# Optimization experiments

Hardware: AMD Instinct MI355X
Metric: run time of the kernel (lower is better)

## Reference

```python
import jax, jax.numpy as jnp
import numpy as np

B, P, K, L, F_NR, KS, NC = 32, 2048, 16, 8, 64, 5, 40
N = B * P
EPS = 1e-5


def setup_inputs() -> dict:
    key = jax.random.key(0)
    ks = jax.random.split(key, 6)
    pos = jax.random.normal(ks[0], (N, 3), jnp.float32)
    batch = jnp.repeat(jnp.arange(B, dtype=jnp.int32), P)
    # SplineConv(1, F_NR, dim=3, kernel_size=KS): weight [KS^3, in=1, out] flattened to [KS^3, F]
    w_spline = jax.random.normal(ks[1], (KS ** 3, F_NR), jnp.float32) * 0.1
    w_root = jax.random.normal(ks[2], (F_NR,), jnp.float32) * 0.1
    b_spline = jnp.zeros((F_NR,), jnp.float32)
    bn_gamma = jnp.ones((F_NR,), jnp.float32)
    bn_beta = jnp.zeros((F_NR,), jnp.float32)
    w1 = jax.random.normal(ks[3], (F_NR, 256), jnp.float32) / np.sqrt(F_NR).astype(np.float32)
    b1 = jnp.zeros((256,), jnp.float32)
    w2 = jax.random.normal(ks[4], (256, NC), jnp.float32) / np.sqrt(256).astype(np.float32)
    b2 = jnp.zeros((NC,), jnp.float32)
    return dict(pos=pos, batch=batch, w_spline=w_spline, w_root=w_root,
                b_spline=b_spline, bn_gamma=bn_gamma, bn_beta=bn_beta,
                w1=w1, b1=b1, w2=w2, b2=b2)


def _knn_one_cloud(pb):  # pb: [P,3] -> k nearest neighbor indices [P,K] (no self loops)
    sq = jnp.sum(pb * pb, axis=-1)
    d = sq[:, None] + sq[None, :] - 2.0 * (pb @ pb.T)
    d = jnp.where(jnp.eye(P, dtype=bool), jnp.inf, d)
    _, idx = jax.lax.top_k(-d, K)
    return idx


def reference(pos, batch, w_spline, w_root, b_spline, bn_gamma, bn_beta, w1, b1, w2, b2):
    # --- knn_graph, grouped k-per-center ---
    posb = pos.reshape(B, P, 3)
    nbr = jax.vmap(_knn_one_cloud)(posb)                          # [B,P,K] local
    nbr = (nbr + (jnp.arange(B) * P)[:, None, None]).reshape(N, K)
    clusters = pos[nbr] - pos[:, None, :]                          # [N,K,3]
    # --- per-point 3x3 covariance over first L neighbors ---
    cl = clusters[:, :L, :]
    cov = jnp.einsum('nlc,nld->ncd', cl, cl)                       # [N,3,3]
    # --- diag(): 5 iterations of batched QR iteration; rows of V = eigenvectors ---
    A = cov
    Vt = jnp.broadcast_to(jnp.eye(3, dtype=pos.dtype), (N, 3, 3))
    for _ in range(5):
        Q, R = jnp.linalg.qr(A)
        A = R @ Q
        Vt = Vt @ Q
    V = jnp.swapaxes(Vt, 1, 2)                                     # [N,3,3]
    # --- rotate clusters into eigenbasis: clusters @ V^T ---
    dc = jnp.einsum('nkc,ndc->nkd', clusters, V)                   # [N,K,3]
    signs = jnp.sign(jnp.sum(dc[:, :, 2], axis=1))
    dc = dc.at[:, :, 2].multiply(signs[:, None])
    max_abs = jnp.max(jnp.abs(dc).reshape(N, K * 3), axis=1)
    dc = dc / max_abs[:, None, None] * 0.5 + 0.5                   # pseudo coords in [0,1]
    # --- SplineConv (degree-1 open B-splines, dim=3): x_j = 1, aggr='mean' ---
    p = dc * (KS - 1)
    i0 = jnp.clip(jnp.floor(p), 0, KS - 2).astype(jnp.int32)       # [N,K,3]
    f = p - i0                                                     # fractional part
    acc = jnp.zeros((N, K, F_NR), pos.dtype)
    for c in range(8):                                             # 8 corners of trilinear basis
        bits = [(c >> d) & 1 for d in range(3)]
        kidx = sum((i0[..., d] + bits[d]) * (KS ** d) for d in range(3))
        w = jnp.ones((N, K), pos.dtype)
        for d in range(3):
            w = w * (f[..., d] if bits[d] else 1.0 - f[..., d])
        acc = acc + w[..., None] * w_spline[kidx]                  # [N,K,F]
    out_nondir = acc.mean(axis=1) + w_root + b_spline              # root*x_i + bias, x_i = 1
    # --- BatchNorm1d (training-mode batch stats, biased var) ---
    mu = out_nondir.mean(axis=0)
    var = out_nondir.var(axis=0)
    y = (out_nondir - mu) / jnp.sqrt(var + EPS) * bn_gamma + bn_beta
    # --- head ---
    y = jax.nn.sigmoid(y)
    ys = y.reshape(B, P, F_NR).mean(axis=1)                        # [B,F]
    y1 = jax.nn.elu(ys @ w1 + b1)
    y2 = jax.nn.log_softmax(y1 @ w2 + b2, axis=1)
    return y2
```

## Files before the change

kernel.cpp:

```cpp
#include <hip/hip_runtime.h>
#include <math.h>

#define B_ 32
#define P_ 2048
#define N_ 65536
#define K_ 16
#define L_ 8
#define F_ 64
#define KS_ 5
#define KS3_ 125
#define NC_ 40
#define H_ 256
#define EPS_ 1e-5f
#define QPB_ 64
#define SEG_ 4
#define SEGLEN_ 512

__device__ __forceinline__ float distf(float4 C, float nx, float ny, float nz, float qs) {
    return fmaf(C.x, nx, fmaf(C.y, ny, fmaf(C.z, nz, C.w))) + qs;
}

#define CES(a, b) { unsigned _mn = min(a, b); b = max(a, b); a = _mn; }

__device__ __forceinline__ void sort8(unsigned& e0, unsigned& e1, unsigned& e2, unsigned& e3,
                                      unsigned& e4, unsigned& e5, unsigned& e6, unsigned& e7) {
    CES(e0, e1) CES(e2, e3) CES(e4, e5) CES(e6, e7)
    CES(e0, e2) CES(e1, e3) CES(e4, e6) CES(e5, e7)
    CES(e1, e2) CES(e5, e6)
    CES(e0, e4) CES(e1, e5) CES(e2, e6) CES(e3, e7)
    CES(e2, e4) CES(e3, e5)
    CES(e1, e2) CES(e3, e4) CES(e5, e6)
}

__device__ __forceinline__ void bitmerge16(unsigned (&a)[16]) {
#pragma unroll
    for (int dd = 8; dd >= 1; dd >>= 1)
#pragma unroll
        for (int k2 = 0; k2 < 16; k2 += 2 * dd)
#pragma unroll
            for (int i2 = k2; i2 < k2 + dd; i2++)
                CES(a[i2], a[i2 + dd])
}

__device__ __forceinline__ void sort16(unsigned (&a)[16]) {
    sort8(a[0], a[1], a[2], a[3], a[4], a[5], a[6], a[7]);
    sort8(a[8], a[9], a[10], a[11], a[12], a[13], a[14], a[15]);
    unsigned t;
    t = a[8];  a[8]  = a[15]; a[15] = t;
    t = a[9];  a[9]  = a[14]; a[14] = t;
    t = a[10]; a[10] = a[13]; a[13] = t;
    t = a[11]; a[11] = a[12]; a[12] = t;
    bitmerge16(a);
}

__device__ __forceinline__ void flush8(unsigned (&bu)[16],
                                       unsigned& e0, unsigned& e1, unsigned& e2, unsigned& e3,
                                       unsigned& e4, unsigned& e5, unsigned& e6, unsigned& e7,
                                       unsigned& thr) {
    sort8(e0, e1, e2, e3, e4, e5, e6, e7);
    CES(bu[8],  e7) CES(bu[9],  e6) CES(bu[10], e5) CES(bu[11], e4)
    CES(bu[12], e3) CES(bu[13], e2) CES(bu[14], e1) CES(bu[15], e0)
    bitmerge16(bu);
    e0 = e1 = e2 = e3 = e4 = e5 = e6 = e7 = 0xFFFFFFFFu;
    unsigned t16 = bu[15];
    t16 = min(t16, (unsigned)__shfl_xor((int)t16, 1, 64));
    t16 = min(t16, (unsigned)__shfl_xor((int)t16, 2, 64));
    thr = min(thr, t16);
}

__global__ __launch_bounds__(256, 4) void knn_geom_kernel(const float* __restrict__ pos,
                                                          float* __restrict__ dcn) {
    __shared__ float4 cloud[P_];
    int b = blockIdx.x >> 5, tile = blockIdx.x & 31;
    int base = b * P_;
    int t = threadIdx.x;
    for (int j = t; j < P_; j += 256) {
        float x = pos[(base + j) * 3 + 0];
        float y = pos[(base + j) * 3 + 1];
        float z = pos[(base + j) * 3 + 2];
        cloud[j] = make_float4(x, y, z, x * x + y * y + z * z);
    }
    __syncthreads();

    int s = t & 3;
    int il = tile * QPB_ + (t >> 2);
    float4 Q = cloud[il];
    float nx = -2.f * Q.x, ny = -2.f * Q.y, nz = -2.f * Q.z, qs = Q.w;

    int j0 = s << 9, off = s << 1;

    unsigned bu[16];
#pragma unroll
    for (int m = 0; m < 16; m++) {
        int j_ = j0 | ((m + off) & 511);
        float4 Cv = cloud[j_];
        float d_ = distf(Cv, nx, ny, nz, qs);
        bu[m] = (__float_as_uint(fmaxf(d_, 0.f)) & 0xFFFFF800u) | (unsigned)j_;
    }
    sort16(bu);
    unsigned thr;
    {
        unsigned t16 = bu[15];
        t16 = min(t16, (unsigned)__shfl_xor((int)t16, 1, 64));
        t16 = min(t16, (unsigned)__shfl_xor((int)t16, 2, 64));
        thr = t16;
    }

    unsigned e0 = ~0u, e1 = ~0u, e2 = ~0u, e3 = ~0u,
             e4 = ~0u, e5 = ~0u, e6 = ~0u, e7 = ~0u;

#define VISIT(Cv, JJ) {                                                          \
        int j_ = j0 | (((JJ) + off) & 511);                                      \
        float d_ = distf(Cv, nx, ny, nz, qs);                                    \
        unsigned key_ = (__float_as_uint(fmaxf(d_, 0.f)) & 0xFFFFF800u)          \
                        | (unsigned)j_;                                          \
        bool a_ = (key_ < thr);                                                  \
        e7 = a_ ? e6 : e7;  e6 = a_ ? e5 : e6;  e5 = a_ ? e4 : e5;               \
        e4 = a_ ? e3 : e4;  e3 = a_ ? e2 : e3;  e2 = a_ ? e1 : e2;               \
        e1 = a_ ? e0 : e1;  e0 = a_ ? key_ : e0;                                 \
    }

    float4 c0 = cloud[j0 | ((16 + off) & 511)];
    float4 c1 = cloud[j0 | ((17 + off) & 511)];
    float4 c2 = cloud[j0 | ((18 + off) & 511)];
    float4 c3 = cloud[j0 | ((19 + off) & 511)];
    for (int jj = 16; jj < SEGLEN_; jj += 4) {
        float4 n0 = cloud[j0 | ((jj + off + 4) & 511)];
        float4 n1 = cloud[j0 | ((jj + off + 5) & 511)];
        float4 n2 = cloud[j0 | ((jj + off + 6) & 511)];
        float4 n3 = cloud[j0 | ((jj + off + 7) & 511)];
        VISIT(c0, jj + 0)
        VISIT(c1, jj + 1)
        VISIT(c2, jj + 2)
        VISIT(c3, jj + 3)
        if (__any(e4 != 0xFFFFFFFFu))
            flush8(bu, e0, e1, e2, e3, e4, e5, e6, e7, thr);
        c0 = n0; c1 = n1; c2 = n2; c3 = n3;
    }
    flush8(bu, e0, e1, e2, e3, e4, e5, e6, e7, thr);
#undef VISIT

    {
        bool own = (s == (il >> 9));
#pragma unroll
        for (int m = 0; m < 15; m++) bu[m] = own ? bu[m + 1] : bu[m];
        bu[15] = own ? 0xFFFFFFFFu : bu[15];
    }

#pragma unroll
    for (int mask = 1; mask <= 2; mask <<= 1) {
        unsigned o[16];
#pragma unroll
        for (int i = 0; i < 16; i++)
            o[i] = (unsigned)__shfl_xor((int)bu[15 - i], mask, 64);
#pragma unroll
        for (int i = 0; i < 16; i++) bu[i] = min(bu[i], o[i]);
        bitmerge16(bu);
    }

    int mi[16];
#pragma unroll
    for (int m = 0; m < 16; m++) mi[m] = bu[m] & 0x7FF;

    float px = Q.x, py = Q.y, pz = Q.z;
    float A[3][3];
    {
        float a00 = 0, a01 = 0, a02 = 0, a11 = 0, a12 = 0, a22 = 0;
#pragma unroll
        for (int l = 0; l < L_; l++) {
            float4 Cv = cloud[mi[l]];
            float ccx = Cv.x - px, ccy = Cv.y - py, ccz = Cv.z - pz;
            a00 += ccx * ccx; a01 += ccx * ccy; a02 += ccx * ccz;
            a11 += ccy * ccy; a12 += ccy * ccz; a22 += ccz * ccz;
        }
        A[0][0] = a00; A[0][1] = a01; A[0][2] = a02;
        A[1][0] = a01; A[1][1] = a11; A[1][2] = a12;
        A[2][0] = a02; A[2][1] = a12; A[2][2] = a22;
    }
    float Vt[3][3] = {{1.f, 0.f, 0.f}, {0.f, 1.f, 0.f}, {0.f, 0.f, 1.f}};

    for (int it = 0; it < 5; it++) {
        float M00 = A[0][0], M01 = A[0][1], M02 = A[0][2];
        float M10 = A[1][0], M11 = A[1][1], M12 = A[1][2];
        float M20 = A[2][0], M21 = A[2][1], M22 = A[2][2];
        float tau0 = 0.f, v1 = 0.f, v2 = 0.f;
        float xn2 = M10 * M10 + M20 * M20;
        if (xn2 != 0.f) {
            float beta = -copysignf(sqrtf(M00 * M00 + xn2), M00);
            tau0 = (beta - M00) / beta;
            float inv = 1.f / (M00 - beta);
            v1 = M10 * inv; v2 = M20 * inv;
            float sc;
            sc = tau0 * (M01 + v1 * M11 + v2 * M21); M01 -= sc; M11 -= v1 * sc; M21 -= v2 * sc;
            sc = tau0 * (M02 + v1 * M12 + v2 * M22); M02 -= sc; M12 -= v1 * sc; M22 -= v2 * sc;
            M00 = beta;
        }
        float tau1 = 0.f, u2 = 0.f;
        if (M21 != 0.f) {
            float beta1 = -copysignf(sqrtf(M11 * M11 + M21 * M21), M11);
            tau1 = (beta1 - M11) / beta1;
            u2 = M21 / (M11 - beta1);
            float sc = tau1 * (M12 + u2 * M22); M12 -= sc; M22 -= u2 * sc;
            M11 = beta1;
        }
        float h11 = 1.f - tau1, h12 = -tau1 * u2, h22 = 1.f - tau1 * u2 * u2;
        float Qm[3][3];
        Qm[0][0] = 1.f - tau0;
        Qm[1][0] = -v1 * tau0;
        Qm[2][0] = -v2 * tau0;
        float t1 = tau0 * (v1 * h11 + v2 * h12);
        Qm[0][1] = -t1;
        Qm[1][1] = h11 - v1 * t1;
        Qm[2][1] = h12 - v2 * t1;
        float t2 = tau0 * (v1 * h12 + v2 * h22);
        Qm[0][2] = -t2;
        Qm[1][2] = h12 - v1 * t2;
        Qm[2][2] = h22 - v2 * t2;
        A[0][0] = M00 * Qm[0][0] + M01 * Qm[1][0] + M02 * Qm[2][0];
        A[0][1] = M00 * Qm[0][1] + M01 * Qm[1][1] + M02 * Qm[2][1];
        A[0][2] = M00 * Qm[0][2] + M01 * Qm[1][2] + M02 * Qm[2][2];
        A[1][0] = M11 * Qm[1][0] + M12 * Qm[2][0];
        A[1][1] = M11 * Qm[1][1] + M12 * Qm[2][1];
        A[1][2] = M11 * Qm[1][2] + M12 * Qm[2][2];
        A[2][0] = M22 * Qm[2][0];
        A[2][1] = M22 * Qm[2][1];
        A[2][2] = M22 * Qm[2][2];
        float nv[3][3];
#pragma unroll
        for (int r = 0; r < 3; r++)
#pragma unroll
            for (int cc = 0; cc < 3; cc++)
                nv[r][cc] = Vt[r][0] * Qm[0][cc] + Vt[r][1] * Qm[1][cc] + Vt[r][2] * Qm[2][cc];
#pragma unroll
        for (int r = 0; r < 3; r++)
#pragma unroll
            for (int cc = 0; cc < 3; cc++) Vt[r][cc] = nv[r][cc];
    }

    float s2 = 0.f, mx01 = 0.f, mx2 = 0.f;
#pragma unroll
    for (int k = 0; k < K_; k++) {
        float4 Cv = cloud[mi[k]];
        float ccx = Cv.x - px, ccy = Cv.y - py, ccz = Cv.z - pz;
        float d0 = ccx * Vt[0][0] + ccy * Vt[1][0] + ccz * Vt[2][0];
        float d1 = ccx * Vt[0][1] + ccy * Vt[1][1] + ccz * Vt[2][1];
        float d2 = ccx * Vt[0][2] + ccy * Vt[1][2] + ccz * Vt[2][2];
        s2 += d2;
        mx01 = fmaxf(mx01, fmaxf(fabsf(d0), fabsf(d1)));
        mx2  = fmaxf(mx2, fabsf(d2));
    }
    float sg = (s2 > 0.f) ? 1.f : ((s2 < 0.f) ? -1.f : 0.f);
    float mx = fmaxf(mx01, (sg == 0.f) ? 0.f : mx2);
    float hs = 0.5f / mx;

    {
        int i = base + il;
        float4* row = (float4*)(dcn + (size_t)i * 48);
        int g = s;
        float v[12];
#pragma unroll
        for (int kk = 0; kk < 4; kk++) {
            int k = g * 4 + kk;
            float4 Cv = cloud[mi[k]];
            float ccx = Cv.x - px, ccy = Cv.y - py, ccz = Cv.z - pz;
            float d0 = ccx * Vt[0][0] + ccy * Vt[1][0] + ccz * Vt[2][0];
            float d1 = ccx * Vt[0][1] + ccy * Vt[1][1] + ccz * Vt[2][1];
            float d2 = (ccx * Vt[0][2] + ccy * Vt[1][2] + ccz * Vt[2][2]) * sg;
            v[kk * 3 + 0] = d0 * hs + 0.5f;
            v[kk * 3 + 1] = d1 * hs + 0.5f;
            v[kk * 3 + 2] = d2 * hs + 0.5f;
        }
#pragma unroll
        for (int r = 0; r < 3; r++)
            row[g * 3 + r] = make_float4(v[r * 4 + 0], v[r * 4 + 1],
                                         v[r * 4 + 2], v[r * 4 + 3]);
    }
}

__global__ __launch_bounds__(256) void spline_kernel(const float* __restrict__ dcn,
                                                     const float* __restrict__ w_spline,
                                                     const float* __restrict__ w_root,
                                                     const float* __restrict__ b_spline,
                                                     float* __restrict__ x,
                                                     float* __restrict__ partials) {
    __shared__ float ws_t[F_ * KS3_];
    __shared__ float red[4][64];
    {
        int f = threadIdx.x & 63;
        for (int c = threadIdx.x >> 6; c < KS3_; c += 4)
            ws_t[f * KS3_ + c] = w_spline[c * 64 + f];
    }
    __syncthreads();
    int wave = threadIdx.x >> 6, f = threadIdx.x & 63;
    const float* wbase = &ws_t[f * KS3_];
    float wr = w_root[f] + b_spline[f];
    float s1 = 0.f, s2 = 0.f;
    for (int p = 0; p < 16; p++) {
        int i = blockIdx.x * 64 + wave * 16 + p;
        const float4* row = (const float4*)(dcn + (size_t)i * 48);
        float pr[48];
#pragma unroll
        for (int m = 0; m < 12; m++) {
            float4 v = row[m];
            pr[m * 4 + 0] = v.x; pr[m * 4 + 1] = v.y;
            pr[m * 4 + 2] = v.z; pr[m * 4 + 3] = v.w;
        }
        float acc = 0.f;
#pragma unroll
        for (int k = 0; k < K_; k++) {
            float p0 = pr[k * 3 + 0] * 4.f;
            float p1 = pr[k * 3 + 1] * 4.f;
            float p2 = pr[k * 3 + 2] * 4.f;
            float i0 = fminf(fmaxf(floorf(p0), 0.f), 3.f);
            float i1 = fminf(fmaxf(floorf(p1), 0.f), 3.f);
            float i2 = fminf(fmaxf(floorf(p2), 0.f), 3.f);
            float f0 = p0 - i0, f1 = p1 - i1, f2 = p2 - i2;
            float g0 = 1.f - f0, g1 = 1.f - f1, g2 = 1.f - f2;
            int c = (int)fmaf(i2, 25.f, fmaf(i1, 5.f, i0));
            const float* wp = wbase + c;
            float a0 = wp[0],  a1 = wp[1];
            float b0 = wp[5],  b1v = wp[6];
            float c0 = wp[25], c1 = wp[26];
            float d0 = wp[30], d1 = wp[31];
            float wA = g1 * g2, wB = f1 * g2, wC = g1 * f2, wD = f1 * f2;
            acc = fmaf(wA, fmaf(f0, a1, g0 * a0), acc);
            acc = fmaf(wB, fmaf(f0, b1v, g0 * b0), acc);
            acc = fmaf(wC, fmaf(f0, c1, g0 * c0), acc);
            acc = fmaf(wD, fmaf(f0, d1, g0 * d0), acc);
        }
        float xv = acc * (1.f / 16.f) + wr;
        x[(size_t)i * 64 + f] = xv;
        s1 += xv; s2 += xv * xv;
    }
    red[wave][f] = s1; __syncthreads();
    if (threadIdx.x < 64)
        partials[blockIdx.x * 128 + f] = red[0][f] + red[1][f] + red[2][f] + red[3][f];
    __syncthreads();
    red[wave][f] = s2; __syncthreads();
    if (threadIdx.x < 64)
        partials[blockIdx.x * 128 + 64 + f] = red[0][f] + red[1][f] + red[2][f] + red[3][f];
}

__global__ __launch_bounds__(256) void stats_kernel(const float* __restrict__ partials,
                                                    const float* __restrict__ gamma,
                                                    const float* __restrict__ beta,
                                                    float* __restrict__ stats) {
    __shared__ double red1[256], red2[256];
    int t = threadIdx.x;
    int f = t & 63, g = t >> 6;
    double a0 = 0, a1 = 0, a2 = 0, a3 = 0, q0 = 0, q1 = 0, q2 = 0, q3 = 0;
    for (int b2 = g; b2 < 1024; b2 += 16) {
        a0 += (double)partials[(b2     ) * 128 + f];
        q0 += (double)partials[(b2     ) * 128 + 64 + f];
        a1 += (double)partials[(b2 +  4) * 128 + f];
        q1 += (double)partials[(b2 +  4) * 128 + 64 + f];
        a2 += (double)partials[(b2 +  8) * 128 + f];
        q2 += (double)partials[(b2 +  8) * 128 + 64 + f];
        a3 += (double)partials[(b2 + 12) * 128 + f];
        q3 += (double)partials[(b2 + 12) * 128 + 64 + f];
    }
    red1[t] = (a0 + a1) + (a2 + a3);
    red2[t] = (q0 + q1) + (q2 + q3);
    __syncthreads();
    if (t < 64) {
        double S1 = red1[t] + red1[t + 64] + red1[t + 128] + red1[t + 192];
        double S2 = red2[t] + red2[t + 64] + red2[t + 128] + red2[t + 192];
        double mu = S1 / (double)N_;
        double var = S2 / (double)N_ - mu * mu;
        double scale = (double)gamma[t] / sqrt(var + (double)EPS_);
        double shift = (double)beta[t] - mu * scale;
        stats[t] = (float)scale;
        stats[64 + t] = (float)shift;
    }
}

__global__ __launch_bounds__(256) void pool_partial_kernel(const float* __restrict__ x,
                                                           const float* __restrict__ stats,
                                                           float* __restrict__ pp) {
    __shared__ float red[4][64];
    int blk = blockIdx.x;
    int b = blk >> 5, ch = blk & 31;
    int f = threadIdx.x & 63, w = threadIdx.x >> 6;
    float scale = stats[f], shift = stats[64 + f];
    float acc = 0.f;
    int row0 = b * P_ + ch * 64;
    for (int r = w; r < 64; r += 4) {
        float v = x[(size_t)(row0 + r) * 64 + f];
        float t = fmaf(v, scale, shift);
        acc += __fdividef(1.f, 1.f + __expf(-t));
    }
    red[w][f] = acc; __syncthreads();
    if (threadIdx.x < 64) pp[blk * 64 + f] = red[0][f] + red[1][f] + red[2][f] + red[3][f];
}

__global__ __launch_bounds__(256) void mlp1_kernel(const float* __restrict__ pp,
                                                   const float* __restrict__ w1,
                                                   const float* __restrict__ b1,
                                                   float* __restrict__ y1) {
    __shared__ float ssy[64];
    int b = blockIdx.x, t = threadIdx.x;
    if (t < 64) {
        float s = 0.f;
#pragma unroll
        for (int g = 0; g < 32; g++) s += pp[(b * 32 + g) * 64 + t];
        ssy[t] = s * (1.f / 2048.f);
    }
    __syncthreads();
    float acc = b1[t];
#pragma unroll 8
    for (int c = 0; c < F_; c++) acc = fmaf(ssy[c], w1[c * 256 + t], acc);
    y1[b * 256 + t] = acc > 0.f ? acc : expm1f(acc);
}

__global__ __launch_bounds__(64) void mlp2_kernel(const float* __restrict__ y1,
                                                  const float* __restrict__ w2,
                                                  const float* __restrict__ b2,
                                                  float* __restrict__ out) {
    int b = blockIdx.x, j = threadIdx.x;
    float acc = -INFINITY;
    if (j < NC_) {
        acc = b2[j];
#pragma unroll 8
        for (int c = 0; c < H_; c++) acc = fmaf(y1[b * 256 + c], w2[c * 40 + j], acc);
    }
    float m = acc;
#pragma unroll
    for (int o = 32; o > 0; o >>= 1) m = fmaxf(m, __shfl_xor(m, o, 64));
    float e = (j < NC_) ? expf(acc - m) : 0.f;
    float s = e;
#pragma unroll
    for (int o = 32; o > 0; o >>= 1) s += __shfl_xor(s, o, 64);
    if (j < NC_) out[b * NC_ + j] = acc - m - logf(s);
}

extern "C" void kernel_launch(void* const* d_in, const int* in_sizes, int n_in,
                              void* d_out, int out_size, void* d_ws, size_t ws_size,
                              hipStream_t stream) {
    const float* pos      = (const float*)d_in[0];
    const float* w_spline = (const float*)d_in[2];
    const float* w_root   = (const float*)d_in[3];
    const float* b_spline = (const float*)d_in[4];
    const float* bn_gamma = (const float*)d_in[5];
    const float* bn_beta  = (const float*)d_in[6];
    const float* w1       = (const float*)d_in[7];
    const float* b1       = (const float*)d_in[8];
    const float* w2       = (const float*)d_in[9];
    const float* b2       = (const float*)d_in[10];
    float* out = (float*)d_out;

    char* ws = (char*)d_ws;
    float* dcn      = (float*)(ws + 0);
    float* x        = (float*)(ws + (12u << 20));
    float* partials = (float*)(ws + (28u << 20));
    float* stats    = (float*)(ws + (28u << 20) + (512u << 10));
    float* pp       = (float*)(ws + (28u << 20) + (512u << 10) + 4096);
    float* y1       = (float*)(ws + (28u << 20) + (512u << 10) + 4096 + (256u << 10));

    knn_geom_kernel<<<B_ * 32, 256, 0, stream>>>(pos, dcn);
    spline_kernel<<<N_ / 64, 256, 0, stream>>>(dcn, w_spline, w_root, b_spline, x, partials);
    stats_kernel<<<1, 256, 0, stream>>>(partials, bn_gamma, bn_beta, stats);
    pool_partial_kernel<<<B_ * 32, 256, 0, stream>>>(x, stats, pp);
    mlp1_kernel<<<B_, 256, 0, stream>>>(pp, w1, b1, y1);
    mlp2_kernel<<<B_, 64, 0, stream>>>(y1, w2, b2, out);
}
```

Measured before the change: 208.1 us.

## Linearize kNN scan addressing with padded cloud and fuse MLP head kernels

The kNN scan loop drops the masked wraparound index computation. It walks a linear pointer with a tail that handles the wrapped-around start elements under predication, and pads the shared cloud with sentinel points so reads past the segment stay in bounds. The neighbor index array is removed in favor of masking the sorted keys directly, and the output projection is rewritten without a temp array. The two small MLP kernels are fused into one so the hidden activations stay in shared memory, which removes a launch and a global round trip. The tail logic adds complexity and risks edge-case errors in how the wrapped elements are covered.

Measured after the change: 192.1 us. -7.7%, faster.

```diff
diff --git a/kernel.cpp b/kernel.cpp
--- a/kernel.cpp
+++ b/kernel.cpp
@@ -14,7 +14,6 @@
 #define EPS_ 1e-5f
 #define QPB_ 64
 #define SEG_ 4
-#define SEGLEN_ 512
 
 __device__ __forceinline__ float distf(float4 C, float nx, float ny, float nz, float qs) {
     return fmaf(C.x, nx, fmaf(C.y, ny, fmaf(C.z, nz, C.w))) + qs;
@@ -70,7 +69,7 @@
 
 __global__ __launch_bounds__(256, 4) void knn_geom_kernel(const float* __restrict__ pos,
                                                           float* __restrict__ dcn) {
-    __shared__ float4 cloud[P_];
+    __shared__ float4 cloud[P_ + 8];
     int b = blockIdx.x >> 5, tile = blockIdx.x & 31;
     int base = b * P_;
     int t = threadIdx.x;
@@ -80,6 +79,7 @@
         float z = pos[(base + j) * 3 + 2];
         cloud[j] = make_float4(x, y, z, x * x + y * y + z * z);
     }
+    if (t < 8) cloud[P_ + t] = make_float4(0.f, 0.f, 0.f, 1e30f);
     __syncthreads();
 
     int s = t & 3;
@@ -92,7 +92,7 @@
     unsigned bu[16];
 #pragma unroll
     for (int m = 0; m < 16; m++) {
-        int j_ = j0 | ((m + off) & 511);
+        int j_ = j0 + off + m;
         float4 Cv = cloud[j_];
         float d_ = distf(Cv, nx, ny, nz, qs);
         bu[m] = (__float_as_uint(fmaxf(d_, 0.f)) & 0xFFFFF800u) | (unsigned)j_;
@@ -109,36 +109,71 @@
     unsigned e0 = ~0u, e1 = ~0u, e2 = ~0u, e3 = ~0u,
              e4 = ~0u, e5 = ~0u, e6 = ~0u, e7 = ~0u;
 
-#define VISIT(Cv, JJ) {                                                          \
-        int j_ = j0 | (((JJ) + off) & 511);                                      \
+#define VISITL(Cv, Jv) {                                                         \
         float d_ = distf(Cv, nx, ny, nz, qs);                                    \
         unsigned key_ = (__float_as_uint(fmaxf(d_, 0.f)) & 0xFFFFF800u)          \
-                        | (unsigned)j_;                                          \
+                        | (unsigned)(Jv);                                        \
         bool a_ = (key_ < thr);                                                  \
         e7 = a_ ? e6 : e7;  e6 = a_ ? e5 : e6;  e5 = a_ ? e4 : e5;               \
         e4 = a_ ? e3 : e4;  e3 = a_ ? e2 : e3;  e2 = a_ ? e1 : e2;               \
         e1 = a_ ? e0 : e1;  e0 = a_ ? key_ : e0;                                 \
     }
-
-    float4 c0 = cloud[j0 | ((16 + off) & 511)];
-    float4 c1 = cloud[j0 | ((17 + off) & 511)];
-    float4 c2 = cloud[j0 | ((18 + off) & 511)];
-    float4 c3 = cloud[j0 | ((19 + off) & 511)];
-    for (int jj = 16; jj < SEGLEN_; jj += 4) {
-        float4 n0 = cloud[j0 | ((jj + off + 4) & 511)];
-        float4 n1 = cloud[j0 | ((jj + off + 5) & 511)];
-        float4 n2 = cloud[j0 | ((jj + off + 6) & 511)];
-        float4 n3 = cloud[j0 | ((jj + off + 7) & 511)];
-        VISIT(c0, jj + 0)
-        VISIT(c1, jj + 1)
-        VISIT(c2, jj + 2)
-        VISIT(c3, jj + 3)
+#define VISITP(Cv, Jv, P) {                                                      \
+        float d_ = distf(Cv, nx, ny, nz, qs);                                    \
+        unsigned key_ = (__float_as_uint(fmaxf(d_, 0.f)) & 0xFFFFF800u)          \
+                        | (unsigned)(Jv);                                        \
+        bool a_ = (key_ < thr) && (P);                                           \
+        e7 = a_ ? e6 : e7;  e6 = a_ ? e5 : e6;  e5 = a_ ? e4 : e5;               \
+        e4 = a_ ? e3 : e4;  e3 = a_ ? e2 : e3;  e2 = a_ ? e1 : e2;               \
+        e1 = a_ ? e0 : e1;  e0 = a_ ? key_ : e0;                                 \
+    }
+
+    const float4* cp = &cloud[j0 + off + 16];
+    int jc = j0 + off + 16;
+    for (int v = 0; v < 488; v += 4) {
+        float4 a0 = cp[v + 0], a1 = cp[v + 1], a2 = cp[v + 2], a3 = cp[v + 3];
+        VISITL(a0, jc + 0)
+        VISITL(a1, jc + 1)
+        VISITL(a2, jc + 2)
+        VISITL(a3, jc + 3)
+        jc += 4;
         if (__any(e4 != 0xFFFFFFFFu))
             flush8(bu, e0, e1, e2, e3, e4, e5, e6, e7, thr);
-        c0 = n0; c1 = n1; c2 = n2; c3 = n3;
+    }
+    {
+        int vlim = 496 - off;
+#pragma unroll
+        for (int v = 488; v < 492; v++) {
+            float4 a0 = cp[v];
+            VISITP(a0, jc, v < vlim) jc++;
+        }
+        if (__any(e4 != 0xFFFFFFFFu))
+            flush8(bu, e0, e1, e2, e3, e4, e5, e6, e7, thr);
+#pragma unroll
+        for (int v = 492; v < 496; v++) {
+            float4 a0 = cp[v];
+            VISITP(a0, jc, v < vlim) jc++;
+        }
+        if (__any(e4 != 0xFFFFFFFFu))
+            flush8(bu, e0, e1, e2, e3, e4, e5, e6, e7, thr);
+    }
+    {
+#pragma unroll
+        for (int u = 0; u < 4; u++) {
+            float4 a0 = cloud[j0 + u];
+            VISITP(a0, j0 + u, u < off)
+        }
+        if (__any(e4 != 0xFFFFFFFFu))
+            flush8(bu, e0, e1, e2, e3, e4, e5, e6, e7, thr);
+#pragma unroll
+        for (int u = 4; u < 6; u++) {
+            float4 a0 = cloud[j0 + u];
+            VISITP(a0, j0 + u, u < off)
+        }
     }
     flush8(bu, e0, e1, e2, e3, e4, e5, e6, e7, thr);
-#undef VISIT
+#undef VISITL
+#undef VISITP
 
     {
         bool own = (s == (il >> 9));
@@ -158,17 +193,13 @@
         bitmerge16(bu);
     }
 
-    int mi[16];
-#pragma unroll
-    for (int m = 0; m < 16; m++) mi[m] = bu[m] & 0x7FF;
-
     float px = Q.x, py = Q.y, pz = Q.z;
     float A[3][3];
     {
         float a00 = 0, a01 = 0, a02 = 0, a11 = 0, a12 = 0, a22 = 0;
 #pragma unroll
         for (int l = 0; l < L_; l++) {
-            float4 Cv = cloud[mi[l]];
+            float4 Cv = cloud[bu[l] & 0x7FF];
             float ccx = Cv.x - px, ccy = Cv.y - py, ccz = Cv.z - pz;
             a00 += ccx * ccx; a01 += ccx * ccy; a02 += ccx * ccz;
             a11 += ccy * ccy; a12 += ccy * ccz; a22 += ccz * ccz;
@@ -240,7 +271,7 @@
     float s2 = 0.f, mx01 = 0.f, mx2 = 0.f;
 #pragma unroll
     for (int k = 0; k < K_; k++) {
-        float4 Cv = cloud[mi[k]];
+        float4 Cv = cloud[bu[k] & 0x7FF];
         float ccx = Cv.x - px, ccy = Cv.y - py, ccz = Cv.z - pz;
         float d0 = ccx * Vt[0][0] + ccy * Vt[1][0] + ccz * Vt[2][0];
         float d1 = ccx * Vt[0][1] + ccy * Vt[1][1] + ccz * Vt[2][1];
@@ -257,23 +288,29 @@
         int i = base + il;
         float4* row = (float4*)(dcn + (size_t)i * 48);
         int g = s;
-        float v[12];
-#pragma unroll
-        for (int kk = 0; kk < 4; kk++) {
-            int k = g * 4 + kk;
-            float4 Cv = cloud[mi[k]];
-            float ccx = Cv.x - px, ccy = Cv.y - py, ccz = Cv.z - pz;
-            float d0 = ccx * Vt[0][0] + ccy * Vt[1][0] + ccz * Vt[2][0];
-            float d1 = ccx * Vt[0][1] + ccy * Vt[1][1] + ccz * Vt[2][1];
-            float d2 = (ccx * Vt[0][2] + ccy * Vt[1][2] + ccz * Vt[2][2]) * sg;
-            v[kk * 3 + 0] = d0 * hs + 0.5f;
-            v[kk * 3 + 1] = d1 * hs + 0.5f;
-            v[kk * 3 + 2] = d2 * hs + 0.5f;
-        }
-#pragma unroll
-        for (int r = 0; r < 3; r++)
-            row[g * 3 + r] = make_float4(v[r * 4 + 0], v[r * 4 + 1],
-                                         v[r * 4 + 2], v[r * 4 + 3]);
+        float4 Cv0 = cloud[bu[g * 4 + 0] & 0x7FF];
+        float4 Cv1 = cloud[bu[g * 4 + 1] & 0x7FF];
+        float4 Cv2 = cloud[bu[g * 4 + 2] & 0x7FF];
+        float4 Cv3 = cloud[bu[g * 4 + 3] & 0x7FF];
+        float x0 = Cv0.x - px, y0 = Cv0.y - py, z0 = Cv0.z - pz;
+        float x1 = Cv1.x - px, y1 = Cv1.y - py, z1 = Cv1.z - pz;
+        float x2 = Cv2.x - px, y2 = Cv2.y - py, z2 = Cv2.z - pz;
+        float x3 = Cv3.x - px, y3 = Cv3.y - py, z3 = Cv3.z - pz;
+        float p00 = (x0 * Vt[0][0] + y0 * Vt[1][0] + z0 * Vt[2][0]) * hs + 0.5f;
+        float p01 = (x0 * Vt[0][1] + y0 * Vt[1][1] + z0 * Vt[2][1]) * hs + 0.5f;
+        float p02 = (x0 * Vt[0][2] + y0 * Vt[1][2] + z0 * Vt[2][2]) * sg * hs + 0.5f;
+        float p10 = (x1 * Vt[0][0] + y1 * Vt[1][0] + z1 * Vt[2][0]) * hs + 0.5f;
+        float p11 = (x1 * Vt[0][1] + y1 * Vt[1][1] + z1 * Vt[2][1]) * hs + 0.5f;
+        float p12 = (x1 * Vt[0][2] + y1 * Vt[1][2] + z1 * Vt[2][2]) * sg * hs + 0.5f;
+        float p20 = (x2 * Vt[0][0] + y2 * Vt[1][0] + z2 * Vt[2][0]) * hs + 0.5f;
+        float p21 = (x2 * Vt[0][1] + y2 * Vt[1][1] + z2 * Vt[2][1]) * hs + 0.5f;
+        float p22 = (x2 * Vt[0][2] + y2 * Vt[1][2] + z2 * Vt[2][2]) * sg * hs + 0.5f;
+        float p30 = (x3 * Vt[0][0] + y3 * Vt[1][0] + z3 * Vt[2][0]) * hs + 0.5f;
+        float p31 = (x3 * Vt[0][1] + y3 * Vt[1][1] + z3 * Vt[2][1]) * hs + 0.5f;
+        float p32 = (x3 * Vt[0][2] + y3 * Vt[1][2] + z3 * Vt[2][2]) * sg * hs + 0.5f;
+        row[g * 3 + 0] = make_float4(p00, p01, p02, p10);
+        row[g * 3 + 1] = make_float4(p11, p12, p20, p21);
+        row[g * 3 + 2] = make_float4(p22, p30, p31, p32);
     }
 }
 
@@ -393,11 +430,14 @@
     if (threadIdx.x < 64) pp[blk * 64 + f] = red[0][f] + red[1][f] + red[2][f] + red[3][f];
 }
 
-__global__ __launch_bounds__(256) void mlp1_kernel(const float* __restrict__ pp,
-                                                   const float* __restrict__ w1,
-                                                   const float* __restrict__ b1,
-                                                   float* __restrict__ y1) {
+__global__ __launch_bounds__(256) void mlp_kernel(const float* __restrict__ pp,
+                                                  const float* __restrict__ w1,
+                                                  const float* __restrict__ b1,
+                                                  const float* __restrict__ w2,
+                                                  const float* __restrict__ b2,
+                                                  float* __restrict__ out) {
     __shared__ float ssy[64];
+    __shared__ float sy1[256];
     int b = blockIdx.x, t = threadIdx.x;
     if (t < 64) {
         float s = 0.f;
@@ -406,31 +446,30 @@
         ssy[t] = s * (1.f / 2048.f);
     }
     __syncthreads();
-    float acc = b1[t];
+    {
+        float acc = b1[t];
 #pragma unroll 8
-    for (int c = 0; c < F_; c++) acc = fmaf(ssy[c], w1[c * 256 + t], acc);
-    y1[b * 256 + t] = acc > 0.f ? acc : expm1f(acc);
-}
-
-__global__ __launch_bounds__(64) void mlp2_kernel(const float* __restrict__ y1,
-                                                  const float* __restrict__ w2,
-                                                  const float* __restrict__ b2,
-                                                  float* __restrict__ out) {
-    int b = blockIdx.x, j = threadIdx.x;
-    float acc = -INFINITY;
-    if (j < NC_) {
-        acc = b2[j];
+        for (int c = 0; c < F_; c++) acc = fmaf(ssy[c], w1[c * 256 + t], acc);
+        sy1[t] = acc > 0.f ? acc : expm1f(acc);
+    }
+    __syncthreads();
+    if (t < 64) {
+        int j = t;
+        float acc = -INFINITY;
+        if (j < NC_) {
+            acc = b2[j];
 #pragma unroll 8
-        for (int c = 0; c < H_; c++) acc = fmaf(y1[b * 256 + c], w2[c * 40 + j], acc);
-    }
-    float m = acc;
-#pragma unroll
-    for (int o = 32; o > 0; o >>= 1) m = fmaxf(m, __shfl_xor(m, o, 64));
-    float e = (j < NC_) ? expf(acc - m) : 0.f;
-    float s = e;
-#pragma unroll
-    for (int o = 32; o > 0; o >>= 1) s += __shfl_xor(s, o, 64);
-    if (j < NC_) out[b * NC_ + j] = acc - m - logf(s);
+            for (int c = 0; c < H_; c++) acc = fmaf(sy1[c], w2[c * 40 + j], acc);
+        }
+        float m = acc;
+#pragma unroll
+        for (int o = 32; o > 0; o >>= 1) m = fmaxf(m, __shfl_xor(m, o, 64));
+        float e = (j < NC_) ? expf(acc - m) : 0.f;
+        float s = e;
+#pragma unroll
+        for (int o = 32; o > 0; o >>= 1) s += __shfl_xor(s, o, 64);
+        if (j < NC_) out[b * NC_ + j] = acc - m - logf(s);
+    }
 }
 
 extern "C" void kernel_launch(void* const* d_in, const int* in_sizes, int n_in,
@@ -454,12 +493,10 @@
     float* partials = (float*)(ws + (28u << 20));
     float* stats    = (float*)(ws + (28u << 20) + (512u << 10));
     float* pp       = (float*)(ws + (28u << 20) + (512u << 10) + 4096);
-    float* y1       = (float*)(ws + (28u << 20) + (512u << 10) + 4096 + (256u << 10));
 
     knn_geom_kernel<<<B_ * 32, 256, 0, stream>>>(pos, dcn);
     spline_kernel<<<N_ / 64, 256, 0, stream>>>(dcn, w_spline, w_root, b_spline, x, partials);
     stats_kernel<<<1, 256, 0, stream>>>(partials, bn_gamma, bn_beta, stats);
     pool_partial_kernel<<<B_ * 32, 256, 0, stream>>>(x, stats, pp);
-    mlp1_kernel<<<B_, 256, 0, stream>>>(pp, w1, b1, y1);
-    mlp2_kernel<<<B_, 64, 0, stream>>>(y1, w2, b2, out);
-}
+    mlp_kernel<<<B_, 256, 0, stream>>>(pp, w1, b1, w2, b2, out);
+}
```
